# Kernel tuning notes

Hardware: AMD Instinct MI355X
Metric: run time of the kernel (lower is better)

Reference implementation:

```python
import jax, jax.numpy as jnp
import numpy as np

N_EMBD = 1024
N_HEAD = 16
HEAD = N_EMBD // N_HEAD


def setup_inputs() -> dict:
    key = jax.random.key(0)
    k1, k2, k3 = jax.random.split(key, 3)
    x = jax.random.normal(k1, (2, 2048, N_EMBD), dtype=jnp.float32)
    # torch Linear weight is [out, in]; store transposed for x @ W
    W_attn = jax.random.normal(k2, (N_EMBD, 3 * N_EMBD), dtype=jnp.float32) * (1.0 / np.sqrt(N_EMBD))
    W_proj = jax.random.normal(k3, (N_EMBD, N_EMBD), dtype=jnp.float32) * (1.0 / np.sqrt(N_EMBD))
    return {"x": x, "W_attn": W_attn, "W_proj": W_proj}


def reference(x, W_attn, W_proj):
    B, T, C = x.shape
    qkv = x @ W_attn  # [B,T,3C]
    q, k, v = jnp.split(qkv, 3, axis=-1)
    # [B,T,H,D] -> [B,H,T,D]
    q = q.reshape(B, T, N_HEAD, HEAD).transpose(0, 2, 1, 3)
    k = k.reshape(B, T, N_HEAD, HEAD).transpose(0, 2, 1, 3)
    v = v.reshape(B, T, N_HEAD, HEAD).transpose(0, 2, 1, 3)
    att = jnp.einsum('bhqd,bhkd->bhqk', q, k) * (1.0 / np.sqrt(HEAD))
    causal = jnp.tril(jnp.ones((T, T), dtype=bool))
    att = jnp.where(causal[None, None], att, jnp.float32(-jnp.inf))
    att = jax.nn.softmax(att, axis=-1)
    y = jnp.einsum('bhqk,bhkd->bhqd', att, v)
    y = y.transpose(0, 2, 1, 3).reshape(B, T, C)
    return y @ W_proj
```

## Files before the change

### kernel.cpp

```cpp
#include <hip/hip_runtime.h>

typedef unsigned short u16;
typedef __bf16 bf16x8 __attribute__((ext_vector_type(8)));
typedef float f32x4 __attribute__((ext_vector_type(4)));

#define BB 2
#define TT 2048
#define CC 1024
#define HH 16
#define DD 64
#define MM (BB*TT)

__device__ __forceinline__ u16 f2b(float f) {
    union { float f; unsigned int i; } a; a.f = f;
    unsigned int u = a.i;
    unsigned int r = (u + 0x7FFFu + ((u >> 16) & 1u)) >> 16;
    return (u16)r;
}
__device__ __forceinline__ u16 f2b_fast(float f) {
    union { float f; unsigned int i; } a; a.f = f;
    return (u16)((a.i + 0x8000u) >> 16);
}

__device__ __forceinline__ void gld16(const u16* g, u16* l) {
    __builtin_amdgcn_global_load_lds(
        (const __attribute__((address_space(1))) unsigned int*)g,
        (__attribute__((address_space(3))) unsigned int*)l, 16, 0, 0);
}

__global__ __launch_bounds__(256) void prep_k(const float* __restrict__ x,
                                              u16* __restrict__ xb,
                                              const float* __restrict__ Wa,
                                              u16* __restrict__ Wat,
                                              const float* __restrict__ Wp,
                                              u16* __restrict__ Wpt) {
    __shared__ u16 tile[64][65];
    const int b = blockIdx.x;
    const int tid = threadIdx.x;
    if (b < 4096) {
        int i = b * 256 + tid;
        float4 v = ((const float4*)x)[i];
        ushort4 o;
        o.x = f2b(v.x); o.y = f2b(v.y); o.z = f2b(v.z); o.w = f2b(v.w);
        ((ushort4*)xb)[i] = o;
        return;
    }
    const float* in; u16* out; int K, N, n0, k0;
    if (b < 4096 + 768) {
        int bb = b - 4096;
        in = Wa; out = Wat; K = 1024; N = 3072;
        n0 = (bb % 48) * 64; k0 = (bb / 48) * 64;
    } else {
        int bb = b - 4096 - 768;
        in = Wp; out = Wpt; K = 1024; N = 1024;
        n0 = (bb % 16) * 64; k0 = (bb / 16) * 64;
    }
    const int tx = tid & 63, ty = tid >> 6;
    for (int i = 0; i < 16; i++) {
        int row = ty + i * 4;
        tile[row][tx] = f2b(in[(size_t)(k0 + row) * N + n0 + tx]);
    }
    __syncthreads();
    for (int i = 0; i < 16; i++) {
        int row = ty + i * 4;
        out[(size_t)(n0 + row) * K + k0 + tx] = tile[tx][row];
    }
}

template<int MODE>
__global__ __launch_bounds__(256) void gemm_k(const u16* __restrict__ A,
                                              const u16* __restrict__ Bt,
                                              u16* __restrict__ Cq,
                                              u16* __restrict__ Ck,
                                              u16* __restrict__ Cv,
                                              float* __restrict__ Cout,
                                              int N, int K) {
    constexpr int BN   = (MODE == 0) ? 128 : 64;
    constexpr int NF   = (MODE == 0) ? 4 : 2;
    constexpr int BSU  = BN * 32;
    constexpr int LDSZ = (MODE == 0) ? (128 * 136) : (2 * 4096 + 2 * BSU);
    __shared__ __attribute__((aligned(16))) u16 smem[LDSZ];
#define AsP(B) (smem + (B) * 4096)
#define BsP(B) (smem + 8192 + (B) * BSU)

    const int tid  = threadIdx.x;
    const int lane = tid & 63, w = tid >> 6;
    const int wm = w >> 1, wn = w & 1;
    const int quad = lane >> 4, l16 = lane & 15;
    const int swg  = (l16 >> 1) & 3;
    const int rsl  = (quad ^ swg) * 8;

    const int nwg = gridDim.x, lin = blockIdx.x;
    const int cpx = nwg >> 3;
    const int sw  = (lin & 7) * cpx + (lin >> 3);
    const int ncols = N / BN;
    const int m0 = (sw / ncols) * 128, n0 = (sw % ncols) * BN;

    f32x4 acc[4][NF];
    for (int mi = 0; mi < 4; mi++)
        for (int ni = 0; ni < NF; ni++)
            for (int e = 0; e < 4; e++) acc[mi][ni][e] = 0.f;

#define GSTAGE(BUF, K0) do {                                                  \
    for (int i = 0; i < 2; i++) {                                             \
        int c = tid + 256 * i;                                                \
        int row = c >> 2, sg = c & 3;                                         \
        int g8 = ((sg ^ ((row >> 1) & 3)) * 8);                               \
        if constexpr (MODE == 0) {                                            \
            gld16(A + (size_t)(m0 + row) * K + (K0) + g8, AsP(BUF) + c * 8);  \
        } else {                                                              \
            int m = m0 + row;                                                 \
            int b = m >> 11, t = m & 2047;                                    \
            int kk = (K0) + g8;                                               \
            int h = kk >> 6, d = kk & 63;                                     \
            gld16(A + ((size_t)(b * HH + h) * TT + t) * DD + d,               \
                  AsP(BUF) + c * 8);                                          \
        }                                                                     \
    }                                                                         \
    if constexpr (MODE == 0) {                                                \
        for (int i = 0; i < 2; i++) {                                         \
            int c = tid + 256 * i;                                            \
            int row = c >> 2;                                                 \
            int g = (c & 3) ^ ((row >> 1) & 3);                               \
            gld16(Bt + (size_t)(n0 + row) * K + (K0) + g * 8,                 \
                  BsP(BUF) + c * 8);                                          \
        }                                                                     \
    } else {                                                                  \
        int row = tid >> 2;                                                   \
        int g = (tid & 3) ^ ((row >> 1) & 3);                                 \
        gld16(Bt + (size_t)(n0 + row) * K + (K0) + g * 8,                     \
              BsP(BUF) + tid * 8);                                            \
    }                                                                         \
} while (0)

    GSTAGE(0, 0);
    const int nk = K >> 5;
    for (int jk = 0; jk < nk; jk++) {
        const int cb = jk & 1;
        __syncthreads();
        if (jk + 1 < nk) { GSTAGE(cb ^ 1, (jk + 1) * 32); }
        bf16x8 af[4], bfm[NF];
        for (int mi = 0; mi < 4; mi++)
            af[mi] = *(const bf16x8*)(AsP(cb) + (wm * 64 + mi * 16 + l16) * 32 + rsl);
        for (int ni = 0; ni < NF; ni++)
            bfm[ni] = *(const bf16x8*)(BsP(cb) + ((BN / 2) * wn + ni * 16 + l16) * 32 + rsl);
        for (int mi = 0; mi < 4; mi++)
            for (int ni = 0; ni < NF; ni++)
                acc[mi][ni] = __builtin_amdgcn_mfma_f32_16x16x32_bf16(
                    af[mi], bfm[ni], acc[mi][ni], 0, 0, 0);
    }
#undef GSTAGE

    if constexpr (MODE == 0) {
        const float SCQ = 0.125f * 1.44269504f;
        const int which = n0 >> 10;
        if (which < 2) {
            for (int mi = 0; mi < 4; mi++)
                for (int ni = 0; ni < 4; ni++)
                    for (int r = 0; r < 4; r++) {
                        int row = m0 + wm * 64 + mi * 16 + quad * 4 + r;
                        int col = n0 + wn * 64 + ni * 16 + l16;
                        int h = (col >> 6) & 15, d = col & 63;
                        int b = row >> 11, t = row & 2047;
                        size_t off = ((size_t)(b * HH + h) * TT + t) * DD + d;
                        float val = acc[mi][ni][r];
                        if (which == 0) val *= SCQ;
                        (which == 0 ? Cq : Ck)[off] = f2b(val);
                    }
        } else {
            __syncthreads();
            for (int mi = 0; mi < 4; mi++)
                for (int ni = 0; ni < 4; ni++)
                    for (int r = 0; r < 4; r++) {
                        int cl = wn * 64 + ni * 16 + l16;
                        int tl = wm * 64 + mi * 16 + quad * 4 + r;
                        smem[cl * 136 + tl] = f2b(acc[mi][ni][r]);
                    }
            __syncthreads();
            const int b = m0 >> 11, t0l = m0 & 2047;
            const int c0 = n0 - 2048;
            for (int j = 0; j < 8; j++) {
                int idx = j * 256 + tid;
                int cl = idx >> 4, ch = idx & 15;
                int cg = c0 + cl, h = cg >> 6, d = cg & 63;
                uint4 val = *(const uint4*)&smem[cl * 136 + ch * 8];
                *(uint4*)&Cv[((size_t)(b * HH + h) * DD + d) * TT + t0l + ch * 8] = val;
            }
        }
    } else {
        for (int mi = 0; mi < 4; mi++)
            for (int ni = 0; ni < NF; ni++)
                for (int r = 0; r < 4; r++) {
                    int row = m0 + wm * 64 + mi * 16 + quad * 4 + r;
                    int col = n0 + wn * 32 + ni * 16 + l16;
                    Cout[(size_t)row * N + col] = acc[mi][ni][r];
                }
    }
#undef AsP
#undef BsP
}

__global__ __launch_bounds__(256, 2) void attn_k(const u16* __restrict__ Q,
                                                 const u16* __restrict__ Kb,
                                                 const u16* __restrict__ Vtg,
                                                 u16* __restrict__ Y) {
    __shared__ __attribute__((aligned(16))) u16 Ks[128 * 64];
    __shared__ __attribute__((aligned(16))) u16 Vs[64 * 128];
    __shared__ __attribute__((aligned(16))) u16 Ps[4][16 * 128];
    const int tid  = threadIdx.x;
    const int lane = tid & 63, w = tid >> 6;
    const int quad = lane >> 4, l16 = lane & 15;
    const int bh = blockIdx.x;
    const int y  = blockIdx.y;
    const int rowi = (y >> 1) & 3, coli = y >> 3;
    const int basew = ((coli & 1) ? 9 : 16) - ((coli >> 1) << 3);
    const int work = basew + ((coli & 1) ? rowi : -rowi);
    const int sb = 2 * (work - 1) + (y & 1);
    const int nkt = work;
    const size_t base  = (size_t)bh * TT * DD;
    const size_t baseV = (size_t)bh * DD * TT;

    int ksidx[4], koff[4], voff[4];
    for (int r = 0; r < 4; r++) {
        int sidx = r * 256 + tid;
        ksidx[r] = sidx;
        int kr = sidx >> 3, ksl = sidx & 7;
        koff[r] = kr * 64 + ((ksl ^ (kr & 7)) << 3);
        int vr = sidx >> 4, vsl = sidx & 15;
        voff[r] = vr * TT + ((vsl ^ (vr & 7)) << 3);
    }
    const u16* kg = Kb + base;
    const u16* vg = Vtg + baseV;

    for (int r = 0; r < 4; r++) gld16(kg + koff[r], &Ks[ksidx[r] * 8]);
    for (int r = 0; r < 4; r++) gld16(vg + voff[r], &Vs[ksidx[r] * 8]);

    bf16x8 qf[2];
    for (int kk = 0; kk < 2; kk++)
        qf[kk] = *(const bf16x8*)(Q + base +
            (size_t)(sb * 64 + w * 16 + l16) * DD + kk * 32 + quad * 8);

    const int swx = (l16 & 7);
    const int swk0 = ((quad ^ swx) << 3);
    const int swk1 = (((4 + quad) ^ swx) << 3);

    float lst[4] = {0.f, 0.f, 0.f, 0.f};
    f32x4 oacc[4];
    for (int nd = 0; nd < 4; nd++)
        for (int e = 0; e < 4; e++) oacc[nd][e] = 0.f;

    for (int jk = 0; jk < nkt; jk++) {
        __syncthreads();

        f32x4 s[8];
        for (int ni = 0; ni < 8; ni++)
            for (int e = 0; e < 4; e++) s[ni][e] = 0.f;
        {
            bf16x8 kfa[8];
            for (int ni = 0; ni < 8; ni++)
                kfa[ni] = *(const bf16x8*)&Ks[(ni * 16 + l16) * 64 + swk0];
            for (int ni = 0; ni < 8; ni++)
                s[ni] = __builtin_amdgcn_mfma_f32_16x16x32_bf16(
                    qf[0], kfa[ni], s[ni], 0, 0, 0);
        }
        {
            bf16x8 kfa[8];
            for (int ni = 0; ni < 8; ni++)
                kfa[ni] = *(const bf16x8*)&Ks[(ni * 16 + l16) * 64 + swk1];
            for (int ni = 0; ni < 8; ni++)
                s[ni] = __builtin_amdgcn_mfma_f32_16x16x32_bf16(
                    qf[1], kfa[ni], s[ni], 0, 0, 0);
        }

        if (jk == (sb >> 1)) {
            int row0 = sb * 64 + w * 16 + quad * 4;
            int col0 = jk * 128 + l16;
            for (int ni = 0; ni < 8; ni++)
                for (int r = 0; r < 4; r++)
                    if (col0 + ni * 16 > row0 + r) s[ni][r] = -1e30f;
        }
        for (int ni = 0; ni < 8; ni++)
            for (int r = 0; r < 4; r++) {
                float pv = __builtin_amdgcn_exp2f(s[ni][r]);
                lst[r] += pv;
                int row = quad * 4 + r;
                int cg  = ni * 2 + (l16 >> 3);
                Ps[w][row * 128 + ((cg ^ row) << 3) + (l16 & 7)] = f2b_fast(pv);
            }

        for (int kk = 0; kk < 4; kk++) {
            const int swv = (((kk * 4 + quad) ^ swx) << 3);
            bf16x8 vfa[4];
            for (int nd = 0; nd < 4; nd++)
                vfa[nd] = *(const bf16x8*)&Vs[(nd * 16 + l16) * 128 + swv];
            bf16x8 pf = *(const bf16x8*)&Ps[w][l16 * 128 +
                (((kk * 4 + quad) ^ l16) << 3)];
            for (int nd = 0; nd < 4; nd++)
                oacc[nd] = __builtin_amdgcn_mfma_f32_16x16x32_bf16(
                    pf, vfa[nd], oacc[nd], 0, 0, 0);
        }

        if (jk + 1 < nkt) {
            __syncthreads();
            const u16* kn = kg + (size_t)(jk + 1) * (128 * DD);
            const u16* vn = vg + (size_t)(jk + 1) * 128;
            for (int r = 0; r < 4; r++)
                gld16(kn + koff[r], &Ks[ksidx[r] * 8]);
            for (int r = 0; r < 4; r++)
                gld16(vn + voff[r], &Vs[ksidx[r] * 8]);
        }
    }

    for (int r = 0; r < 4; r++)
        for (int off = 8; off >= 1; off >>= 1)
            lst[r] += __shfl_xor(lst[r], off);

    for (int nd = 0; nd < 4; nd++)
        for (int r = 0; r < 4; r++) {
            int row = sb * 64 + w * 16 + quad * 4 + r;
            int col = nd * 16 + l16;
            Y[base + (size_t)row * DD + col] = f2b(oacc[nd][r] / lst[r]);
        }
}

extern "C" void kernel_launch(void* const* d_in, const int* in_sizes, int n_in,
                              void* d_out, int out_size, void* d_ws, size_t ws_size,
                              hipStream_t stream) {
    const float* x      = (const float*)d_in[0];
    const float* W_attn = (const float*)d_in[1];
    const float* W_proj = (const float*)d_in[2];
    float* out = (float*)d_out;

    u16* Wt_attn = (u16*)d_ws;
    u16* Wt_proj = Wt_attn + 3072 * 1024;
    u16* xb      = Wt_proj + 1024 * 1024;
    u16* q       = xb + (size_t)MM * CC;
    u16* k       = q + (size_t)32 * 2048 * 64;
    u16* vt      = k + (size_t)32 * 2048 * 64;
    u16* y       = vt + (size_t)32 * 2048 * 64;

    prep_k<<<dim3(4096 + 768 + 256), 256, 0, stream>>>(
        x, xb, W_attn, Wt_attn, W_proj, Wt_proj);
    gemm_k<0><<<dim3((MM / 128) * (3072 / 128)), 256, 0, stream>>>(
        xb, Wt_attn, q, k, vt, nullptr, 3072, 1024);
    attn_k<<<dim3(32, 32), 256, 0, stream>>>(q, k, vt, y);
    gemm_k<1><<<dim3((MM / 128) * (1024 / 64)), 256, 0, stream>>>(
        y, Wt_proj, nullptr, nullptr, nullptr, out, 1024, 1024);
}
```

Baseline: 167.1 us.

## Compute transposed S tile and feed P to PV MFMA via shuffles instead of LDS

The QK^T MFMA operands are swapped so each lane holds a column of the score tile (keys by query), which lets probabilities be packed into bf16 pairs in registers. The P operand for the PV MFMA is then rebuilt with cross-lane shuffles rather than being written to and read back from a per-wave LDS buffer. This removes the Ps shared array, its scalar stores and its reads, and cuts the row-sum reduction to a few shuffles. In exchange it adds eight ds_bpermute shuffles plus selects per k-chunk, and changes the masking and normalisation indexing.

```diff
diff --git a/kernel.cpp b/kernel.cpp
--- a/kernel.cpp
+++ b/kernel.cpp
@@ -1,6 +1,7 @@
 #include <hip/hip_runtime.h>
 
 typedef unsigned short u16;
+typedef unsigned int u32;
 typedef __bf16 bf16x8 __attribute__((ext_vector_type(8)));
 typedef float f32x4 __attribute__((ext_vector_type(4)));
 
@@ -20,6 +21,9 @@
 __device__ __forceinline__ u16 f2b_fast(float f) {
     union { float f; unsigned int i; } a; a.f = f;
     return (u16)((a.i + 0x8000u) >> 16);
+}
+__device__ __forceinline__ u32 pack2(float lo, float hi) {
+    return ((u32)f2b_fast(hi) << 16) | (u32)f2b_fast(lo);
 }
 
 __device__ __forceinline__ void gld16(const u16* g, u16* l) {
@@ -206,7 +210,6 @@
                                                  u16* __restrict__ Y) {
     __shared__ __attribute__((aligned(16))) u16 Ks[128 * 64];
     __shared__ __attribute__((aligned(16))) u16 Vs[64 * 128];
-    __shared__ __attribute__((aligned(16))) u16 Ps[4][16 * 128];
     const int tid  = threadIdx.x;
     const int lane = tid & 63, w = tid >> 6;
     const int quad = lane >> 4, l16 = lane & 15;
@@ -244,7 +247,11 @@
     const int swk0 = ((quad ^ swx) << 3);
     const int swk1 = (((4 + quad) ^ swx) << 3);
 
-    float lst[4] = {0.f, 0.f, 0.f, 0.f};
+    const int qg   = sb * 64 + w * 16 + l16;
+    const int srcA = ((quad & 1) << 5) + l16;
+    const int hi   = quad >> 1;
+
+    float lsum = 0.f;
     f32x4 oacc[4];
     for (int nd = 0; nd < 4; nd++)
         for (int e = 0; e < 4; e++) oacc[nd][e] = 0.f;
@@ -252,52 +259,63 @@
     for (int jk = 0; jk < nkt; jk++) {
         __syncthreads();
 
-        f32x4 s[8];
+        f32x4 sT[8];
         for (int ni = 0; ni < 8; ni++)
-            for (int e = 0; e < 4; e++) s[ni][e] = 0.f;
+            for (int e = 0; e < 4; e++) sT[ni][e] = 0.f;
         {
             bf16x8 kfa[8];
             for (int ni = 0; ni < 8; ni++)
                 kfa[ni] = *(const bf16x8*)&Ks[(ni * 16 + l16) * 64 + swk0];
             for (int ni = 0; ni < 8; ni++)
-                s[ni] = __builtin_amdgcn_mfma_f32_16x16x32_bf16(
-                    qf[0], kfa[ni], s[ni], 0, 0, 0);
+                sT[ni] = __builtin_amdgcn_mfma_f32_16x16x32_bf16(
+                    kfa[ni], qf[0], sT[ni], 0, 0, 0);
         }
         {
             bf16x8 kfa[8];
             for (int ni = 0; ni < 8; ni++)
                 kfa[ni] = *(const bf16x8*)&Ks[(ni * 16 + l16) * 64 + swk1];
             for (int ni = 0; ni < 8; ni++)
-                s[ni] = __builtin_amdgcn_mfma_f32_16x16x32_bf16(
-                    qf[1], kfa[ni], s[ni], 0, 0, 0);
+                sT[ni] = __builtin_amdgcn_mfma_f32_16x16x32_bf16(
+                    kfa[ni], qf[1], sT[ni], 0, 0, 0);
         }
 
         if (jk == (sb >> 1)) {
-            int row0 = sb * 64 + w * 16 + quad * 4;
-            int col0 = jk * 128 + l16;
+            int kb0 = jk * 128 + quad * 4;
             for (int ni = 0; ni < 8; ni++)
                 for (int r = 0; r < 4; r++)
-                    if (col0 + ni * 16 > row0 + r) s[ni][r] = -1e30f;
-        }
-        for (int ni = 0; ni < 8; ni++)
-            for (int r = 0; r < 4; r++) {
-                float pv = __builtin_amdgcn_exp2f(s[ni][r]);
-                lst[r] += pv;
-                int row = quad * 4 + r;
-                int cg  = ni * 2 + (l16 >> 3);
-                Ps[w][row * 128 + ((cg ^ row) << 3) + (l16 & 7)] = f2b_fast(pv);
-            }
+                    if (kb0 + ni * 16 + r > qg) sT[ni][r] = -1e30f;
+        }
+
+        u32 pd[8][2];
+        for (int ni = 0; ni < 8; ni++) {
+            float p0 = __builtin_amdgcn_exp2f(sT[ni][0]);
+            float p1 = __builtin_amdgcn_exp2f(sT[ni][1]);
+            float p2 = __builtin_amdgcn_exp2f(sT[ni][2]);
+            float p3 = __builtin_amdgcn_exp2f(sT[ni][3]);
+            lsum += (p0 + p1) + (p2 + p3);
+            pd[ni][0] = pack2(p0, p1);
+            pd[ni][1] = pack2(p2, p3);
+        }
 
         for (int kk = 0; kk < 4; kk++) {
             const int swv = (((kk * 4 + quad) ^ swx) << 3);
             bf16x8 vfa[4];
             for (int nd = 0; nd < 4; nd++)
                 vfa[nd] = *(const bf16x8*)&Vs[(nd * 16 + l16) * 128 + swv];
-            bf16x8 pf = *(const bf16x8*)&Ps[w][l16 * 128 +
-                (((kk * 4 + quad) ^ l16) << 3)];
+            u32 a0 = pd[2 * kk][0],     a1 = pd[2 * kk][1];
+            u32 b0 = pd[2 * kk + 1][0], b1 = pd[2 * kk + 1][1];
+            u32 t0 = __shfl((int)a0, srcA),      t1 = __shfl((int)a1, srcA);
+            u32 t2 = __shfl((int)a0, srcA + 16), t3 = __shfl((int)a1, srcA + 16);
+            u32 u0 = __shfl((int)b0, srcA),      u1 = __shfl((int)b1, srcA);
+            u32 u2 = __shfl((int)b0, srcA + 16), u3 = __shfl((int)b1, srcA + 16);
+            union { u32 d[4]; bf16x8 v; } pf;
+            pf.d[0] = hi ? u0 : t0;
+            pf.d[1] = hi ? u1 : t1;
+            pf.d[2] = hi ? u2 : t2;
+            pf.d[3] = hi ? u3 : t3;
             for (int nd = 0; nd < 4; nd++)
                 oacc[nd] = __builtin_amdgcn_mfma_f32_16x16x32_bf16(
-                    pf, vfa[nd], oacc[nd], 0, 0, 0);
+                    pf.v, vfa[nd], oacc[nd], 0, 0, 0);
         }
 
         if (jk + 1 < nkt) {
@@ -311,15 +329,17 @@
         }
     }
 
+    lsum += __shfl_xor(lsum, 16);
+    lsum += __shfl_xor(lsum, 32);
+    float lsty[4];
     for (int r = 0; r < 4; r++)
-        for (int off = 8; off >= 1; off >>= 1)
-            lst[r] += __shfl_xor(lst[r], off);
+        lsty[r] = __shfl(lsum, quad * 4 + r);
 
     for (int nd = 0; nd < 4; nd++)
         for (int r = 0; r < 4; r++) {
             int row = sb * 64 + w * 16 + quad * 4 + r;
             int col = nd * 16 + l16;
-            Y[base + (size_t)row * DD + col] = f2b(oacc[nd][r] / lst[r]);
+            Y[base + (size_t)row * DD + col] = f2b(oacc[nd][r] / lsty[r]);
         }
 }
 
```

Result: no change. 166.0 us (-0.6%).

## Pair complementary causal query blocks per workgroup and pass P via shuffles

Applied to the files above, without the earlier changes.

Each attention workgroup now processes two query blocks (31-p and p), so every K/V tile loaded into LDS serves both, and the causal work per block is balanced without the old index remapping. Scores are computed transposed (K as the A operand), and the probabilities are packed to bf16 and moved into MFMA A-operand layout with cross-lane shuffles instead of a round trip through shared memory. The row-sum reduction changes to match. This halves the grid and adds register pressure from two accumulator sets, which may lower occupancy under the 2-wave launch bound.

```diff
diff --git a/kernel.cpp b/kernel.cpp
--- a/kernel.cpp
+++ b/kernel.cpp
@@ -1,6 +1,7 @@
 #include <hip/hip_runtime.h>
 
 typedef unsigned short u16;
+typedef unsigned int u32;
 typedef __bf16 bf16x8 __attribute__((ext_vector_type(8)));
 typedef float f32x4 __attribute__((ext_vector_type(4)));
 
@@ -20,6 +21,9 @@
 __device__ __forceinline__ u16 f2b_fast(float f) {
     union { float f; unsigned int i; } a; a.f = f;
     return (u16)((a.i + 0x8000u) >> 16);
+}
+__device__ __forceinline__ u32 pack2(float lo, float hi) {
+    return ((u32)f2b_fast(hi) << 16) | (u32)f2b_fast(lo);
 }
 
 __device__ __forceinline__ void gld16(const u16* g, u16* l) {
@@ -206,17 +210,14 @@
                                                  u16* __restrict__ Y) {
     __shared__ __attribute__((aligned(16))) u16 Ks[128 * 64];
     __shared__ __attribute__((aligned(16))) u16 Vs[64 * 128];
-    __shared__ __attribute__((aligned(16))) u16 Ps[4][16 * 128];
     const int tid  = threadIdx.x;
     const int lane = tid & 63, w = tid >> 6;
     const int quad = lane >> 4, l16 = lane & 15;
     const int bh = blockIdx.x;
-    const int y  = blockIdx.y;
-    const int rowi = (y >> 1) & 3, coli = y >> 3;
-    const int basew = ((coli & 1) ? 9 : 16) - ((coli >> 1) << 3);
-    const int work = basew + ((coli & 1) ? rowi : -rowi);
-    const int sb = 2 * (work - 1) + (y & 1);
-    const int nkt = work;
+    const int p  = blockIdx.y;
+    const int sb0 = 31 - p, sb1 = p;
+    const int nkt0 = (sb0 >> 1) + 1;
+    const int nkt1 = (sb1 >> 1) + 1;
     const size_t base  = (size_t)bh * TT * DD;
     const size_t baseV = (size_t)bh * DD * TT;
 
@@ -235,72 +236,93 @@
     for (int r = 0; r < 4; r++) gld16(kg + koff[r], &Ks[ksidx[r] * 8]);
     for (int r = 0; r < 4; r++) gld16(vg + voff[r], &Vs[ksidx[r] * 8]);
 
-    bf16x8 qf[2];
-    for (int kk = 0; kk < 2; kk++)
-        qf[kk] = *(const bf16x8*)(Q + base +
-            (size_t)(sb * 64 + w * 16 + l16) * DD + kk * 32 + quad * 8);
+    bf16x8 qf0[2], qf1[2];
+    for (int kk = 0; kk < 2; kk++) {
+        qf0[kk] = *(const bf16x8*)(Q + base +
+            (size_t)(sb0 * 64 + w * 16 + l16) * DD + kk * 32 + quad * 8);
+        qf1[kk] = *(const bf16x8*)(Q + base +
+            (size_t)(sb1 * 64 + w * 16 + l16) * DD + kk * 32 + quad * 8);
+    }
 
     const int swx = (l16 & 7);
     const int swk0 = ((quad ^ swx) << 3);
     const int swk1 = (((4 + quad) ^ swx) << 3);
 
-    float lst[4] = {0.f, 0.f, 0.f, 0.f};
-    f32x4 oacc[4];
+    const int qr   = w * 16 + l16;
+    const int srcA = ((quad & 1) << 5) + l16;
+    const int hi   = quad >> 1;
+
+    float lsum0 = 0.f, lsum1 = 0.f;
+    f32x4 oacc0[4], oacc1[4];
     for (int nd = 0; nd < 4; nd++)
-        for (int e = 0; e < 4; e++) oacc[nd][e] = 0.f;
-
-    for (int jk = 0; jk < nkt; jk++) {
+        for (int e = 0; e < 4; e++) { oacc0[nd][e] = 0.f; oacc1[nd][e] = 0.f; }
+
+#define UNIT(QF, OACC, LSUM, SB) do {                                         \
+    f32x4 sT[8];                                                              \
+    for (int ni = 0; ni < 8; ni++)                                            \
+        for (int e = 0; e < 4; e++) sT[ni][e] = 0.f;                          \
+    {                                                                         \
+        bf16x8 kfa[8];                                                        \
+        for (int ni = 0; ni < 8; ni++)                                        \
+            kfa[ni] = *(const bf16x8*)&Ks[(ni * 16 + l16) * 64 + swk0];       \
+        for (int ni = 0; ni < 8; ni++)                                        \
+            sT[ni] = __builtin_amdgcn_mfma_f32_16x16x32_bf16(                 \
+                kfa[ni], QF[0], sT[ni], 0, 0, 0);                             \
+    }                                                                         \
+    {                                                                         \
+        bf16x8 kfa[8];                                                        \
+        for (int ni = 0; ni < 8; ni++)                                        \
+            kfa[ni] = *(const bf16x8*)&Ks[(ni * 16 + l16) * 64 + swk1];       \
+        for (int ni = 0; ni < 8; ni++)                                        \
+            sT[ni] = __builtin_amdgcn_mfma_f32_16x16x32_bf16(                 \
+                kfa[ni], QF[1], sT[ni], 0, 0, 0);                             \
+    }                                                                         \
+    if (jk == ((SB) >> 1)) {                     \
+        int kb0 = jk * 128 + quad * 4;                                        \
+        int qgl = (SB) * 64 + qr;                                             \
+        for (int ni = 0; ni < 8; ni++)                                        \
+            for (int r = 0; r < 4; r++)                                       \
+                if (kb0 + ni * 16 + r > qgl) sT[ni][r] = -1e30f;              \
+    }                                                                         \
+    u32 pd[8][2];                                                             \
+    for (int ni = 0; ni < 8; ni++) {                                          \
+        float p0 = __builtin_amdgcn_exp2f(sT[ni][0]);                         \
+        float p1 = __builtin_amdgcn_exp2f(sT[ni][1]);                         \
+        float p2 = __builtin_amdgcn_exp2f(sT[ni][2]);                         \
+        float p3 = __builtin_amdgcn_exp2f(sT[ni][3]);                         \
+        LSUM += (p0 + p1) + (p2 + p3);                                        \
+        pd[ni][0] = pack2(p0, p1);                                            \
+        pd[ni][1] = pack2(p2, p3);                                            \
+    }                                                                         \
+    for (int kk = 0; kk < 4; kk++) {                                          \
+        const int swv = (((kk * 4 + quad) ^ swx) << 3);                       \
+        bf16x8 vfa[4];                                                        \
+        for (int nd = 0; nd < 4; nd++)                                        \
+            vfa[nd] = *(const bf16x8*)&Vs[(nd * 16 + l16) * 128 + swv];       \
+        u32 a0 = pd[2 * kk][0],     a1 = pd[2 * kk][1];                       \
+        u32 b0 = pd[2 * kk + 1][0], b1 = pd[2 * kk + 1][1];                   \
+        u32 t0 = __shfl((int)a0, srcA),      t1 = __shfl((int)a1, srcA);      \
+        u32 t2 = __shfl((int)a0, srcA + 16), t3 = __shfl((int)a1, srcA + 16); \
+        u32 u0 = __shfl((int)b0, srcA),      u1 = __shfl((int)b1, srcA);      \
+        u32 u2 = __shfl((int)b0, srcA + 16), u3 = __shfl((int)b1, srcA + 16); \
+        union { u32 d[4]; bf16x8 v; } pf;                                     \
+        pf.d[0] = hi ? u0 : t0;                                               \
+        pf.d[1] = hi ? u1 : t1;                                               \
+        pf.d[2] = hi ? u2 : t2;                                               \
+        pf.d[3] = hi ? u3 : t3;                                               \
+        for (int nd = 0; nd < 4; nd++)                                        \
+            OACC[nd] = __builtin_amdgcn_mfma_f32_16x16x32_bf16(               \
+                pf.v, vfa[nd], OACC[nd], 0, 0, 0);                            \
+    }                                                                         \
+} while (0)
+
+    for (int jk = 0; jk < nkt0; jk++) {
         __syncthreads();
 
-        f32x4 s[8];
-        for (int ni = 0; ni < 8; ni++)
-            for (int e = 0; e < 4; e++) s[ni][e] = 0.f;
-        {
-            bf16x8 kfa[8];
-            for (int ni = 0; ni < 8; ni++)
-                kfa[ni] = *(const bf16x8*)&Ks[(ni * 16 + l16) * 64 + swk0];
-            for (int ni = 0; ni < 8; ni++)
-                s[ni] = __builtin_amdgcn_mfma_f32_16x16x32_bf16(
-                    qf[0], kfa[ni], s[ni], 0, 0, 0);
-        }
-        {
-            bf16x8 kfa[8];
-            for (int ni = 0; ni < 8; ni++)
-                kfa[ni] = *(const bf16x8*)&Ks[(ni * 16 + l16) * 64 + swk1];
-            for (int ni = 0; ni < 8; ni++)
-                s[ni] = __builtin_amdgcn_mfma_f32_16x16x32_bf16(
-                    qf[1], kfa[ni], s[ni], 0, 0, 0);
-        }
-
-        if (jk == (sb >> 1)) {
-            int row0 = sb * 64 + w * 16 + quad * 4;
-            int col0 = jk * 128 + l16;
-            for (int ni = 0; ni < 8; ni++)
-                for (int r = 0; r < 4; r++)
-                    if (col0 + ni * 16 > row0 + r) s[ni][r] = -1e30f;
-        }
-        for (int ni = 0; ni < 8; ni++)
-            for (int r = 0; r < 4; r++) {
-                float pv = __builtin_amdgcn_exp2f(s[ni][r]);
-                lst[r] += pv;
-                int row = quad * 4 + r;
-                int cg  = ni * 2 + (l16 >> 3);
-                Ps[w][row * 128 + ((cg ^ row) << 3) + (l16 & 7)] = f2b_fast(pv);
-            }
-
-        for (int kk = 0; kk < 4; kk++) {
-            const int swv = (((kk * 4 + quad) ^ swx) << 3);
-            bf16x8 vfa[4];
-            for (int nd = 0; nd < 4; nd++)
-                vfa[nd] = *(const bf16x8*)&Vs[(nd * 16 + l16) * 128 + swv];
-            bf16x8 pf = *(const bf16x8*)&Ps[w][l16 * 128 +
-                (((kk * 4 + quad) ^ l16) << 3)];
-            for (int nd = 0; nd < 4; nd++)
-                oacc[nd] = __builtin_amdgcn_mfma_f32_16x16x32_bf16(
-                    pf, vfa[nd], oacc[nd], 0, 0, 0);
-        }
-
-        if (jk + 1 < nkt) {
+        UNIT(qf0, oacc0, lsum0, sb0);
+        if (jk < nkt1) UNIT(qf1, oacc1, lsum1, sb1);
+
+        if (jk + 1 < nkt0) {
             __syncthreads();
             const u16* kn = kg + (size_t)(jk + 1) * (128 * DD);
             const u16* vn = vg + (size_t)(jk + 1) * 128;
@@ -310,16 +332,24 @@
                 gld16(vn + voff[r], &Vs[ksidx[r] * 8]);
         }
     }
-
-    for (int r = 0; r < 4; r++)
-        for (int off = 8; off >= 1; off >>= 1)
-            lst[r] += __shfl_xor(lst[r], off);
+#undef UNIT
+
+    lsum0 += __shfl_xor(lsum0, 16);
+    lsum0 += __shfl_xor(lsum0, 32);
+    lsum1 += __shfl_xor(lsum1, 16);
+    lsum1 += __shfl_xor(lsum1, 32);
+    float lsty0[4], lsty1[4];
+    for (int r = 0; r < 4; r++) {
+        lsty0[r] = __shfl(lsum0, quad * 4 + r);
+        lsty1[r] = __shfl(lsum1, quad * 4 + r);
+    }
 
     for (int nd = 0; nd < 4; nd++)
         for (int r = 0; r < 4; r++) {
-            int row = sb * 64 + w * 16 + quad * 4 + r;
+            int rr = w * 16 + quad * 4 + r;
             int col = nd * 16 + l16;
-            Y[base + (size_t)row * DD + col] = f2b(oacc[nd][r] / lst[r]);
+            Y[base + (size_t)(sb0 * 64 + rr) * DD + col] = f2b(oacc0[nd][r] / lsty0[r]);
+            Y[base + (size_t)(sb1 * 64 + rr) * DD + col] = f2b(oacc1[nd][r] / lsty1[r]);
         }
 }
 
@@ -343,7 +373,7 @@
         x, xb, W_attn, Wt_attn, W_proj, Wt_proj);
     gemm_k<0><<<dim3((MM / 128) * (3072 / 128)), 256, 0, stream>>>(
         xb, Wt_attn, q, k, vt, nullptr, 3072, 1024);
-    attn_k<<<dim3(32, 32), 256, 0, stream>>>(q, k, vt, y);
+    attn_k<<<dim3(32, 16), 256, 0, stream>>>(q, k, vt, y);
     gemm_k<1><<<dim3((MM / 128) * (1024 / 64)), 256, 0, stream>>>(
         y, Wt_proj, nullptr, nullptr, nullptr, out, 1024, 1024);
 }
```

Measured after the change: 172.6 us. +3.3%, slower.
